# Optimization experiments

Measured on AMD Instinct MI355X. Metric: run time of the kernel, lower is better.

Reference implementation:

```python
import jax, jax.numpy as jnp
import numpy as np

NUM_HEADS = 16
HEAD_DIM = 64
HIDDEN = NUM_HEADS * HEAD_DIM
LN_EPS = 1e-6


def setup_inputs() -> dict:
    key = jax.random.key(0)
    ks = jax.random.split(key, 5)
    B, T, H = 2, 2048, HIDDEN
    s = 1.0 / np.sqrt(H)
    return {
        "h": jax.random.normal(ks[0], (B, T, H), jnp.float32),
        "Wq": jax.random.normal(ks[1], (H, H), jnp.float32) * s,
        "bq": jnp.zeros((H,), jnp.float32),
        "Wk": jax.random.normal(ks[2], (H, H), jnp.float32) * s,
        "bk": jnp.zeros((H,), jnp.float32),
        "Wv": jax.random.normal(ks[3], (H, H), jnp.float32) * s,
        "bv": jnp.zeros((H,), jnp.float32),
        "Wo": jax.random.normal(ks[4], (H, H), jnp.float32) * s,
        "bo": jnp.zeros((H,), jnp.float32),
        "gamma": jnp.ones((H,), jnp.float32),
        "beta": jnp.zeros((H,), jnp.float32),
    }


def _split_heads(x):
    B, T, H = x.shape
    return x.reshape(B, T, NUM_HEADS, HEAD_DIM).transpose(0, 2, 1, 3)  # [B,h,T,d]


def reference(h, Wq, bq, Wk, bk, Wv, bv, Wo, bo, gamma, beta):
    # QKV projections (nn.Linear: x @ W^T + b)
    Q = _split_heads(h @ Wq.T + bq)
    K = _split_heads(h @ Wk.T + bk)
    V = _split_heads(h @ Wv.T + bv)
    scale = HEAD_DIM ** -0.5
    scores = jnp.einsum("bhqd,bhkd->bhqk", Q, K) * scale  # [B,h,T,T]
    attn = jax.nn.softmax(scores, axis=-1)
    ctx = jnp.einsum("bhqk,bhkd->bhqd", attn, V)          # [B,h,T,d]
    B, _, T, _ = ctx.shape
    ctx = ctx.transpose(0, 2, 1, 3).reshape(B, T, HIDDEN)
    out = ctx @ Wo.T + bo + h  # dropout is identity at eval
    # LayerNorm(eps=1e-6)
    mu = out.mean(-1, keepdims=True)
    var = jnp.mean((out - mu) ** 2, -1, keepdims=True)
    return (out - mu) * jax.lax.rsqrt(var + LN_EPS) * gamma + beta
```

## Files before the change

kernel.cpp:

```cpp
#include <hip/hip_runtime.h>
#include <hip/hip_bf16.h>

#define NH   16
#define HD   64
#define HID  1024
#define TSEQ 2048
#define BATCH 2
#define KSCALE 0.18033688011112042f

typedef __attribute__((ext_vector_type(4))) float f32x4;
typedef __attribute__((ext_vector_type(8))) short s16x8;
typedef __attribute__((ext_vector_type(4))) short s16x4;
typedef __attribute__((ext_vector_type(8))) _Float16 f16x8;
typedef __attribute__((ext_vector_type(4))) _Float16 f16x4;
typedef __attribute__((ext_vector_type(2))) _Float16 f16x2;

__device__ __forceinline__ unsigned short f2bf(float f) {
  union { float f; unsigned int u; } v; v.f = f;
  unsigned int r = v.u + 0x7fffu + ((v.u >> 16) & 1u);
  return (unsigned short)(r >> 16);
}
__device__ __forceinline__ float bf2f(unsigned short b) {
  union { unsigned int u; float f; } v; v.u = ((unsigned int)b) << 16; return v.f;
}

__device__ __forceinline__ void gll16(const void* g, void* l) {
  __builtin_amdgcn_global_load_lds(
      (const __attribute__((address_space(1))) unsigned int*)g,
      (__attribute__((address_space(3))) unsigned int*)l, 16, 0, 0);
}

#define WAITBAR(N)                                                      \
  do {                                                                  \
    __builtin_amdgcn_sched_barrier(0);                                  \
    asm volatile("s_waitcnt vmcnt(" #N ")\n\ts_barrier" ::: "memory");  \
  } while (0)

__global__ __launch_bounds__(256) void cast_all_k(
    const float* __restrict__ h,
    const float* __restrict__ w0, const float* __restrict__ w1,
    const float* __restrict__ w2, const float* __restrict__ w3,
    unsigned short* __restrict__ hb, unsigned short* __restrict__ wbase) {
  int i = blockIdx.x * 256 + threadIdx.x;
  const float* src; unsigned short* dst; int idx; float sc = 1.f;
  if (i < 1048576) { src = h; dst = hb; idx = i; }
  else {
    int idx4 = i - 1048576;
    int w = idx4 >> 18;
    idx = idx4 & 262143;
    src = (w == 0) ? w0 : (w == 1) ? w1 : (w == 2) ? w2 : w3;
    dst = wbase + (size_t)(idx4 - idx) * 4;
    if (w == 1) sc = KSCALE;
  }
  float4 v = ((const float4*)src)[idx];
  ushort4 o;
  o.x = f2bf(v.x * sc); o.y = f2bf(v.y * sc); o.z = f2bf(v.z * sc); o.w = f2bf(v.w * sc);
  ((ushort4*)dst)[idx] = o;
}

__global__ __launch_bounds__(256) void gemm_qkv(
    const unsigned short* __restrict__ hb,
    const unsigned short* __restrict__ wcat,
    const float* __restrict__ bq, const float* __restrict__ bk, const float* __restrict__ bv,
    unsigned short* __restrict__ qo, unsigned short* __restrict__ ko,
    unsigned short* __restrict__ vto) {
  __shared__ unsigned short Ash[4][128 * 32];
  __shared__ unsigned short Bsh[4][192 * 32];
  const int tid = threadIdx.x, lane = tid & 63, wave = tid >> 6;
  const int l15 = lane & 15, quad = lane >> 4;
  const int wr = wave >> 1, wc = wave & 1;
  const int bn = blockIdx.x * 192, bm = blockIdx.y * 128;
  const char* Ab = (const char*)(hb + (size_t)bm * HID);
  const char* Bb = (const char*)(wcat + (size_t)bn * HID);
  const int off = tid * 16;
  const int r0 = off >> 6, c0 = off & 63;
  const size_t ga0 = (size_t)r0 * (HID * 2) + c0;
  const size_t ga1 = ga0 + (size_t)64  * (HID * 2);
  const size_t gb2 = ga0 + (size_t)128 * (HID * 2);
  const int lb0 = wave * 512;
  const int lb1 = 2048 + wave * 512;
  const int lb2 = 4096 + wave * 512;

  f32x4 acc[4][6];
#pragma unroll
  for (int i = 0; i < 4; ++i)
#pragma unroll
    for (int j = 0; j < 6; ++j) acc[i][j] = f32x4{0.f, 0.f, 0.f, 0.f};

  auto stage = [&](int bufi, int k0) {
    const size_t kb = (size_t)k0 * 2;
    gll16(Ab + ga0 + kb, &Ash[bufi][lb0]);
    gll16(Ab + ga1 + kb, &Ash[bufi][lb1]);
    gll16(Bb + ga0 + kb, &Bsh[bufi][lb0]);
    gll16(Bb + ga1 + kb, &Bsh[bufi][lb1]);
    gll16(Bb + gb2 + kb, &Bsh[bufi][lb2]);
  };
  auto compute = [&](int bufi) {
    s16x8 af[4], bfr[6];
#pragma unroll
    for (int i = 0; i < 4; ++i)
      af[i] = *(const s16x8*)(&Ash[bufi][(wr * 64 + i * 16 + l15) * 32 + quad * 8]);
#pragma unroll
    for (int j = 0; j < 6; ++j)
      bfr[j] = *(const s16x8*)(&Bsh[bufi][(wc * 96 + j * 16 + l15) * 32 + quad * 8]);
#pragma unroll
    for (int i = 0; i < 4; ++i)
#pragma unroll
      for (int j = 0; j < 6; ++j)
        acc[i][j] = __builtin_amdgcn_mfma_f32_16x16x32_bf16(af[i], bfr[j], acc[i][j], 0, 0, 0);
  };

  stage(0, 0);
  stage(1, 32);
  stage(2, 64);
  int cur = 0, pf = 3;
  const int NT = HID / 32;
  for (int t = 0; t < NT - 3; ++t) {
    WAITBAR(10);
    stage(pf, (t + 3) * 32);
    compute(cur);
    cur = (cur + 1) & 3;
    pf  = (pf + 1) & 3;
  }
  WAITBAR(10); compute(cur); cur = (cur + 1) & 3;
  WAITBAR(5);  compute(cur); cur = (cur + 1) & 3;
  WAITBAR(0);  compute(cur);

  const int rbase = bm + wr * 64;
#pragma unroll
  for (int j = 0; j < 6; ++j) {
    const int cg  = bn + wc * 96 + j * 16;
    const int mat = cg >> 10;
    const int coln = (cg & 1023) + l15;
    const int head = coln >> 6, d = coln & 63;
    if (mat == 2) {
      const float bb = bv[coln];
#pragma unroll
      for (int i = 0; i < 4; ++i) {
        const int row0 = rbase + i * 16 + quad * 4;
        const int bI = row0 >> 11, t0 = row0 & 2047;
        unsigned short o[4];
#pragma unroll
        for (int r = 0; r < 4; ++r) {
          _Float16 hv = (_Float16)(acc[i][j][r] + bb);
          o[r] = __builtin_bit_cast(unsigned short, hv);
        }
        *(s16x4*)(vto + ((size_t)((bI * NH + head) * HD + d)) * TSEQ + t0) = *(const s16x4*)o;
      }
    } else {
      unsigned short* dst = (mat == 0) ? qo : ko;
      const float bb = (mat == 0) ? bq[coln] : bk[coln] * KSCALE;
#pragma unroll
      for (int i = 0; i < 4; ++i) {
#pragma unroll
        for (int r = 0; r < 4; ++r) {
          const int row = rbase + i * 16 + quad * 4 + r;
          const int bI = row >> 11, t = row & 2047;
          dst[(((size_t)(bI * NH + head) * TSEQ) + t) * HD + d] = f2bf(acc[i][j][r] + bb);
        }
      }
    }
  }
}

__global__ __launch_bounds__(256) void gemm_out(
    const unsigned short* __restrict__ ctx, const unsigned short* __restrict__ wo,
    const float* __restrict__ bo, const float* __restrict__ hres,
    float* __restrict__ outf) {
  __shared__ unsigned short Ash[5][128 * 32];
  __shared__ unsigned short Bsh[5][64 * 32];
  const int tid = threadIdx.x, lane = tid & 63, wave = tid >> 6;
  const int l15 = lane & 15, quad = lane >> 4;
  const int wr = wave >> 1, wc = wave & 1;
  const int bn = blockIdx.x * 64, bm = blockIdx.y * 128;
  const char* Ab = (const char*)(ctx + (size_t)bm * HID);
  const char* Bb = (const char*)(wo + (size_t)bn * HID);
  const int off = tid * 16;
  const int r0 = off >> 6, c0 = off & 63;
  const size_t ga0 = (size_t)r0 * (HID * 2) + c0;
  const size_t ga1 = ga0 + (size_t)64 * (HID * 2);
  const int lb0 = wave * 512, lb1 = 2048 + wave * 512;

  f32x4 acc[4][2];
#pragma unroll
  for (int i = 0; i < 4; ++i)
#pragma unroll
    for (int j = 0; j < 2; ++j) acc[i][j] = f32x4{0.f, 0.f, 0.f, 0.f};

  auto stage = [&](int bufi, int k0) {
    const size_t kb = (size_t)k0 * 2;
    gll16(Ab + ga0 + kb, &Ash[bufi][lb0]);
    gll16(Ab + ga1 + kb, &Ash[bufi][lb1]);
    gll16(Bb + ga0 + kb, &Bsh[bufi][lb0]);
  };
  auto compute = [&](int bufi) {
    s16x8 af[4], bfr[2];
#pragma unroll
    for (int i = 0; i < 4; ++i)
      af[i] = *(const s16x8*)(&Ash[bufi][(wr * 64 + i * 16 + l15) * 32 + quad * 8]);
#pragma unroll
    for (int j = 0; j < 2; ++j)
      bfr[j] = *(const s16x8*)(&Bsh[bufi][(wc * 32 + j * 16 + l15) * 32 + quad * 8]);
#pragma unroll
    for (int i = 0; i < 4; ++i)
#pragma unroll
      for (int j = 0; j < 2; ++j)
        acc[i][j] = __builtin_amdgcn_mfma_f32_16x16x32_bf16(af[i], bfr[j], acc[i][j], 0, 0, 0);
  };

  stage(0, 0);
  stage(1, 32);
  stage(2, 64);
  stage(3, 96);
  int cur = 0, pf = 4;
  const int NT = HID / 32;
  for (int t = 0; t < NT - 4; ++t) {
    WAITBAR(9);
    stage(pf, (t + 4) * 32);
    compute(cur);
    cur = (cur == 4) ? 0 : cur + 1;
    pf  = (pf  == 4) ? 0 : pf + 1;
  }
  WAITBAR(9); compute(cur); cur = (cur == 4) ? 0 : cur + 1;
  WAITBAR(6); compute(cur); cur = (cur == 4) ? 0 : cur + 1;
  WAITBAR(3); compute(cur); cur = (cur == 4) ? 0 : cur + 1;
  WAITBAR(0); compute(cur);

#pragma unroll
  for (int j = 0; j < 2; ++j) {
    const int col = bn + wc * 32 + j * 16 + l15;
    const float bb = bo[col];
#pragma unroll
    for (int i = 0; i < 4; ++i) {
#pragma unroll
      for (int r = 0; r < 4; ++r) {
        const int row = bm + wr * 64 + i * 16 + quad * 4 + r;
        const size_t o = (size_t)row * HID + col;
        outf[o] = acc[i][j][r] + bb + hres[o];
      }
    }
  }
}

__global__ __launch_bounds__(256, 2) void attn_k(
    const unsigned short* __restrict__ qb, const unsigned short* __restrict__ kb,
    const unsigned short* __restrict__ vt, unsigned short* __restrict__ ctx,
    unsigned short* __restrict__ Opart, float* __restrict__ rsumP,
    int lsplit, int ntiles) {
  __shared__ unsigned short Ksh[64 * 72];
  __shared__ unsigned short Vsh[64 * 72];

  const int tid = threadIdx.x, lane = tid & 63, wave = tid >> 6;
  const int l15 = lane & 15, quad = lane >> 4;
  const int z = blockIdx.z;
  const int b = z >> lsplit;
  const int part = z & ((1 << lsplit) - 1);
  const int h = blockIdx.y, qt = blockIdx.x;
  const size_t ho = ((size_t)(b * NH + h)) * TSEQ * HD;
  const unsigned short* Qh = qb + ho;
  const unsigned short* Kh = kb + ho;
  const unsigned short* Vh = vt + ho;
  const int q0 = qt * 128 + wave * 32;
  const int kt0 = part * ntiles;

  s16x8 qf[2][2];
#pragma unroll
  for (int s = 0; s < 2; ++s)
#pragma unroll
    for (int ks = 0; ks < 2; ++ks)
      qf[s][ks] = *(const s16x8*)(Qh + (size_t)(q0 + s * 16 + l15) * HD + ks * 32 + quad * 8);

  f32x4 accO[4][2];
  float rsum[2];
#pragma unroll
  for (int n2 = 0; n2 < 4; ++n2)
#pragma unroll
    for (int s = 0; s < 2; ++s) accO[n2][s] = f32x4{0.f, 0.f, 0.f, 0.f};
  rsum[0] = rsum[1] = 0.f;

  const int sr = tid >> 3, sc = (tid & 7) * 8;
  const int c = tid & 7;
  const int vwb = (c >> 2) * 32 + (c & 1) * 16 + ((c & 3) >> 1) * 4;
  s16x8 kreg[2], vreg[2];
#pragma unroll
  for (int hf = 0; hf < 2; ++hf) {
    kreg[hf] = *(const s16x8*)(Kh + (size_t)(kt0 * 64 + sr + hf * 32) * HD + sc);
    vreg[hf] = *(const s16x8*)(Vh + (size_t)(sr + hf * 32) * TSEQ + kt0 * 64 + sc);
  }

  for (int kt = 0; kt < ntiles; ++kt) {
    __syncthreads();
#pragma unroll
    for (int hf = 0; hf < 2; ++hf) {
      *(s16x8*)(Ksh + (sr + hf * 32) * 72 + sc) = kreg[hf];
      const s16x4* vh = (const s16x4*)&vreg[hf];
      *(s16x4*)(Vsh + (sr + hf * 32) * 72 + vwb)     = vh[0];
      *(s16x4*)(Vsh + (sr + hf * 32) * 72 + vwb + 8) = vh[1];
    }
    __syncthreads();
    if (kt + 1 < ntiles) {
      const int k0n = (kt0 + kt + 1) * 64;
#pragma unroll
      for (int hf = 0; hf < 2; ++hf) {
        kreg[hf] = *(const s16x8*)(Kh + (size_t)(k0n + sr + hf * 32) * HD + sc);
        vreg[hf] = *(const s16x8*)(Vh + (size_t)(sr + hf * 32) * TSEQ + k0n + sc);
      }
    }

    f32x4 accS[2][4];
#pragma unroll
    for (int s = 0; s < 2; ++s)
#pragma unroll
      for (int n = 0; n < 4; ++n) accS[s][n] = f32x4{0.f, 0.f, 0.f, 0.f};
#pragma unroll
    for (int ks = 0; ks < 2; ++ks) {
#pragma unroll
      for (int n = 0; n < 4; ++n) {
        s16x8 kf = *(const s16x8*)(Ksh + (n * 16 + l15) * 72 + ks * 32 + quad * 8);
#pragma unroll
        for (int s = 0; s < 2; ++s)
          accS[s][n] = __builtin_amdgcn_mfma_f32_16x16x32_bf16(kf, qf[s][ks], accS[s][n], 0, 0, 0);
      }
    }

    f16x4 pB[2][4];
#pragma unroll
    for (int s = 0; s < 2; ++s)
#pragma unroll
      for (int n = 0; n < 4; ++n) {
        float e0 = __builtin_amdgcn_exp2f(accS[s][n][0]);
        float e1 = __builtin_amdgcn_exp2f(accS[s][n][1]);
        float e2 = __builtin_amdgcn_exp2f(accS[s][n][2]);
        float e3 = __builtin_amdgcn_exp2f(accS[s][n][3]);
        rsum[s] += (e0 + e1) + (e2 + e3);
        f16x2 lo = __builtin_bit_cast(f16x2, __builtin_amdgcn_cvt_pkrtz(e0, e1));
        f16x2 hi = __builtin_bit_cast(f16x2, __builtin_amdgcn_cvt_pkrtz(e2, e3));
        pB[s][n] = f16x4{lo[0], lo[1], hi[0], hi[1]};
      }

#pragma unroll
    for (int kk = 0; kk < 2; ++kk) {
      union { f16x4 h[2]; f16x8 v8; } u0, u1;
      u0.h[0] = pB[0][2 * kk]; u0.h[1] = pB[0][2 * kk + 1];
      u1.h[0] = pB[1][2 * kk]; u1.h[1] = pB[1][2 * kk + 1];
#pragma unroll
      for (int n2 = 0; n2 < 4; ++n2) {
        f16x8 vA = *(const f16x8*)(Vsh + (n2 * 16 + l15) * 72 + kk * 32 + quad * 8);
        accO[n2][0] = __builtin_amdgcn_mfma_f32_16x16x32_f16(vA, u0.v8, accO[n2][0], 0, 0, 0);
        accO[n2][1] = __builtin_amdgcn_mfma_f32_16x16x32_f16(vA, u1.v8, accO[n2][1], 0, 0, 0);
      }
    }
  }

#pragma unroll
  for (int s = 0; s < 2; ++s) {
    float t = rsum[s];
    t += __shfl_xor(t, 16, 64);
    t += __shfl_xor(t, 32, 64);
    rsum[s] = t;
  }

  if (lsplit) {
    const int slot = (part * BATCH + b) * NH + h;
    const size_t ob = (size_t)slot * TSEQ * HD;
#pragma unroll
    for (int s = 0; s < 2; ++s) {
      const int t = q0 + s * 16 + l15;
#pragma unroll
      for (int n2 = 0; n2 < 4; ++n2) {
        const int d0 = n2 * 16 + quad * 4;
        unsigned short o[4];
#pragma unroll
        for (int r = 0; r < 4; ++r) o[r] = f2bf(accO[n2][s][r]);
        *(s16x4*)(Opart + ob + (size_t)t * HD + d0) = *(const s16x4*)o;
      }
    }
    if (quad == 0) {
      const size_t rb = (size_t)slot * TSEQ;
#pragma unroll
      for (int s = 0; s < 2; ++s)
        rsumP[rb + q0 + s * 16 + l15] = rsum[s];
    }
  } else {
#pragma unroll
    for (int s = 0; s < 2; ++s) {
      const int t = q0 + s * 16 + l15;
      const float inv = 1.f / rsum[s];
#pragma unroll
      for (int n2 = 0; n2 < 4; ++n2) {
        const int d0 = n2 * 16 + quad * 4;
        unsigned short o[4];
#pragma unroll
        for (int r = 0; r < 4; ++r) o[r] = f2bf(accO[n2][s][r] * inv);
        *(s16x4*)(ctx + ((size_t)(b * TSEQ + t)) * HID + h * HD + d0) = *(const s16x4*)o;
      }
    }
  }
}

__global__ __launch_bounds__(256) void combine_k(
    const unsigned short* __restrict__ Opart, const float* __restrict__ rsumP,
    unsigned short* __restrict__ ctx, int nparts) {
  const int gtid = blockIdx.x * 256 + threadIdx.x;
  const int d = (gtid & 7) * 8;
  const int rem = gtid >> 3;
  const int t = rem & 2047;
  const int bh = rem >> 11;
  float acc[8] = {0, 0, 0, 0, 0, 0, 0, 0};
  float rs = 0.f;
  for (int p = 0; p < nparts; ++p) {
    const int slot = p * 32 + bh;
    s16x8 a = *(const s16x8*)(Opart + ((size_t)slot * TSEQ + t) * HD + d);
#pragma unroll
    for (int j = 0; j < 8; ++j) acc[j] += bf2f(((const unsigned short*)&a)[j]);
    rs += rsumP[(size_t)slot * TSEQ + t];
  }
  const float inv = 1.f / rs;
  unsigned short o[8];
#pragma unroll
  for (int j = 0; j < 8; ++j) o[j] = f2bf(acc[j] * inv);
  const int b = bh >> 4, h = bh & 15;
  *(s16x8*)(ctx + ((size_t)(b * TSEQ + t)) * HID + h * HD + d) = *(const s16x8*)o;
}

__global__ __launch_bounds__(256) void ln_k(float* __restrict__ io,
                                            const float* __restrict__ gamma,
                                            const float* __restrict__ beta) {
  const int row = blockIdx.x, tid = threadIdx.x;
  float x[4]; float s = 0.f, s2 = 0.f;
#pragma unroll
  for (int i = 0; i < 4; ++i) {
    x[i] = io[(size_t)row * HID + tid + i * 256];
    s += x[i]; s2 += x[i] * x[i];
  }
#pragma unroll
  for (int off = 1; off < 64; off <<= 1) {
    s  += __shfl_xor(s, off, 64);
    s2 += __shfl_xor(s2, off, 64);
  }
  __shared__ float red[8];
  const int wave = tid >> 6;
  if ((tid & 63) == 0) { red[wave] = s; red[wave + 4] = s2; }
  __syncthreads();
  s  = red[0] + red[1] + red[2] + red[3];
  s2 = red[4] + red[5] + red[6] + red[7];
  const float mean = s * (1.f / HID);
  const float var  = s2 * (1.f / HID) - mean * mean;
  const float rstd = rsqrtf(var + 1e-6f);
#pragma unroll
  for (int i = 0; i < 4; ++i) {
    const int col = tid + i * 256;
    io[(size_t)row * HID + col] = (x[i] - mean) * rstd * gamma[col] + beta[col];
  }
}

extern "C" void kernel_launch(void* const* d_in, const int* in_sizes, int n_in,
                              void* d_out, int out_size, void* d_ws, size_t ws_size,
                              hipStream_t stream) {
  const float* h    = (const float*)d_in[0];
  const float* Wq   = (const float*)d_in[1];
  const float* bq   = (const float*)d_in[2];
  const float* Wk   = (const float*)d_in[3];
  const float* bk   = (const float*)d_in[4];
  const float* Wv   = (const float*)d_in[5];
  const float* bv   = (const float*)d_in[6];
  const float* Wo   = (const float*)d_in[7];
  const float* bo   = (const float*)d_in[8];
  const float* gamma = (const float*)d_in[9];
  const float* beta  = (const float*)d_in[10];
  float* out = (float*)d_out;

  unsigned short* hb   = (unsigned short*)d_ws;
  unsigned short* wqb  = hb  + 4194304;
  unsigned short* wkb  = wqb + 1048576;
  unsigned short* wvb  = wkb + 1048576;
  unsigned short* wob  = wvb + 1048576;
  unsigned short* qb   = wob + 1048576;
  unsigned short* kb   = qb  + 4194304;
  unsigned short* vtf  = kb  + 4194304;
  unsigned short* Opart = vtf + 4194304;
  unsigned short* ctxb = hb;

  const size_t base = (size_t)(vtf + 4194304 - hb) * 2;
  int lsplit = 0;
  if (ws_size >= base + 2u * 8388608 + 2u * 262144) lsplit = 1;
  const int nparts = 1 << lsplit;
  float* rsumP = (float*)(Opart + (size_t)nparts * 4194304);

  cast_all_k<<<8192, 256, 0, stream>>>(h, Wq, Wk, Wv, Wo, hb, wqb);
  gemm_qkv<<<dim3(16, 32), 256, 0, stream>>>(hb, wqb, bq, bk, bv, qb, kb, vtf);
  attn_k<<<dim3(TSEQ / 128, NH, BATCH << lsplit), 256, 0, stream>>>(
      qb, kb, vtf, ctxb, Opart, rsumP, lsplit, 32 >> lsplit);
  if (lsplit)
    combine_k<<<2048, 256, 0, stream>>>(Opart, rsumP, ctxb, nparts);
  gemm_out<<<dim3(16, 32), 256, 0, stream>>>(ctxb, wob, bo, h, out);
  ln_k<<<4096, 256, 0, stream>>>(out, gamma, beta);
}
```

Before: 209.5 us.

## Software-pipeline attention loop with triple-buffered LDS and MFMA row sums

Restructures the attention inner loop into a software pipeline. QK^T for tile t+1 is issued alongside PV for tile t, using three rotating K/V LDS buffers so only one barrier per iteration is needed. The softmax row sum now comes from an extra MFMA against a ones vector instead of scalar adds plus cross-lane shuffles. LDS use triples to about 55KB per block, which may cut occupancy below the launch bound of two blocks. The row sums are also accumulated from fp16-rounded probabilities, which slightly changes precision.

After: 204.3 us. -2.5%, faster.

```diff
diff --git a/kernel.cpp b/kernel.cpp
--- a/kernel.cpp
+++ b/kernel.cpp
@@ -247,8 +247,8 @@
     const unsigned short* __restrict__ vt, unsigned short* __restrict__ ctx,
     unsigned short* __restrict__ Opart, float* __restrict__ rsumP,
     int lsplit, int ntiles) {
-  __shared__ unsigned short Ksh[64 * 72];
-  __shared__ unsigned short Vsh[64 * 72];
+  __shared__ unsigned short Ksh[3][64 * 72];
+  __shared__ unsigned short Vsh[3][64 * 72];
 
   const int tid = threadIdx.x, lane = tid & 63, wave = tid >> 6;
   const int l15 = lane & 15, quad = lane >> 4;
@@ -271,43 +271,42 @@
       qf[s][ks] = *(const s16x8*)(Qh + (size_t)(q0 + s * 16 + l15) * HD + ks * 32 + quad * 8);
 
   f32x4 accO[4][2];
-  float rsum[2];
+  f32x4 accR[2];
 #pragma unroll
   for (int n2 = 0; n2 < 4; ++n2)
 #pragma unroll
     for (int s = 0; s < 2; ++s) accO[n2][s] = f32x4{0.f, 0.f, 0.f, 0.f};
-  rsum[0] = rsum[1] = 0.f;
+  accR[0] = accR[1] = f32x4{0.f, 0.f, 0.f, 0.f};
+  const f16x8 vones = {(_Float16)1.f, (_Float16)1.f, (_Float16)1.f, (_Float16)1.f,
+                       (_Float16)1.f, (_Float16)1.f, (_Float16)1.f, (_Float16)1.f};
 
   const int sr = tid >> 3, sc = (tid & 7) * 8;
   const int c = tid & 7;
   const int vwb = (c >> 2) * 32 + (c & 1) * 16 + ((c & 3) >> 1) * 4;
   s16x8 kreg[2], vreg[2];
-#pragma unroll
-  for (int hf = 0; hf < 2; ++hf) {
-    kreg[hf] = *(const s16x8*)(Kh + (size_t)(kt0 * 64 + sr + hf * 32) * HD + sc);
-    vreg[hf] = *(const s16x8*)(Vh + (size_t)(sr + hf * 32) * TSEQ + kt0 * 64 + sc);
-  }
-
-  for (int kt = 0; kt < ntiles; ++kt) {
-    __syncthreads();
+
+  auto ldregs = [&](int kt) {
+    const int k0n = (kt0 + kt) * 64;
 #pragma unroll
     for (int hf = 0; hf < 2; ++hf) {
-      *(s16x8*)(Ksh + (sr + hf * 32) * 72 + sc) = kreg[hf];
+      kreg[hf] = *(const s16x8*)(Kh + (size_t)(k0n + sr + hf * 32) * HD + sc);
+      vreg[hf] = *(const s16x8*)(Vh + (size_t)(sr + hf * 32) * TSEQ + k0n + sc);
+    }
+  };
+  auto wlds = [&](int bi) {
+#pragma unroll
+    for (int hf = 0; hf < 2; ++hf) {
+      *(s16x8*)(Ksh[bi] + (sr + hf * 32) * 72 + sc) = kreg[hf];
       const s16x4* vh = (const s16x4*)&vreg[hf];
-      *(s16x4*)(Vsh + (sr + hf * 32) * 72 + vwb)     = vh[0];
-      *(s16x4*)(Vsh + (sr + hf * 32) * 72 + vwb + 8) = vh[1];
-    }
-    __syncthreads();
-    if (kt + 1 < ntiles) {
-      const int k0n = (kt0 + kt + 1) * 64;
-#pragma unroll
-      for (int hf = 0; hf < 2; ++hf) {
-        kreg[hf] = *(const s16x8*)(Kh + (size_t)(k0n + sr + hf * 32) * HD + sc);
-        vreg[hf] = *(const s16x8*)(Vh + (size_t)(sr + hf * 32) * TSEQ + k0n + sc);
-      }
-    }
-
-    f32x4 accS[2][4];
+      *(s16x4*)(Vsh[bi] + (sr + hf * 32) * 72 + vwb)     = vh[0];
+      *(s16x4*)(Vsh[bi] + (sr + hf * 32) * 72 + vwb + 8) = vh[1];
+    }
+  };
+
+  f32x4 accS[2][4];
+  f16x4 pP[2][4];
+
+  auto qkt = [&](int bi) {
 #pragma unroll
     for (int s = 0; s < 2; ++s)
 #pragma unroll
@@ -316,14 +315,14 @@
     for (int ks = 0; ks < 2; ++ks) {
 #pragma unroll
       for (int n = 0; n < 4; ++n) {
-        s16x8 kf = *(const s16x8*)(Ksh + (n * 16 + l15) * 72 + ks * 32 + quad * 8);
+        s16x8 kf = *(const s16x8*)(Ksh[bi] + (n * 16 + l15) * 72 + ks * 32 + quad * 8);
 #pragma unroll
         for (int s = 0; s < 2; ++s)
           accS[s][n] = __builtin_amdgcn_mfma_f32_16x16x32_bf16(kf, qf[s][ks], accS[s][n], 0, 0, 0);
       }
     }
-
-    f16x4 pB[2][4];
+  };
+  auto expp = [&]() {
 #pragma unroll
     for (int s = 0; s < 2; ++s)
 #pragma unroll
@@ -332,33 +331,48 @@
         float e1 = __builtin_amdgcn_exp2f(accS[s][n][1]);
         float e2 = __builtin_amdgcn_exp2f(accS[s][n][2]);
         float e3 = __builtin_amdgcn_exp2f(accS[s][n][3]);
-        rsum[s] += (e0 + e1) + (e2 + e3);
         f16x2 lo = __builtin_bit_cast(f16x2, __builtin_amdgcn_cvt_pkrtz(e0, e1));
         f16x2 hi = __builtin_bit_cast(f16x2, __builtin_amdgcn_cvt_pkrtz(e2, e3));
-        pB[s][n] = f16x4{lo[0], lo[1], hi[0], hi[1]};
-      }
-
+        pP[s][n] = f16x4{lo[0], lo[1], hi[0], hi[1]};
+      }
+  };
+  auto pv = [&](int bi) {
 #pragma unroll
     for (int kk = 0; kk < 2; ++kk) {
       union { f16x4 h[2]; f16x8 v8; } u0, u1;
-      u0.h[0] = pB[0][2 * kk]; u0.h[1] = pB[0][2 * kk + 1];
-      u1.h[0] = pB[1][2 * kk]; u1.h[1] = pB[1][2 * kk + 1];
+      u0.h[0] = pP[0][2 * kk]; u0.h[1] = pP[0][2 * kk + 1];
+      u1.h[0] = pP[1][2 * kk]; u1.h[1] = pP[1][2 * kk + 1];
+      accR[0] = __builtin_amdgcn_mfma_f32_16x16x32_f16(vones, u0.v8, accR[0], 0, 0, 0);
+      accR[1] = __builtin_amdgcn_mfma_f32_16x16x32_f16(vones, u1.v8, accR[1], 0, 0, 0);
 #pragma unroll
       for (int n2 = 0; n2 < 4; ++n2) {
-        f16x8 vA = *(const f16x8*)(Vsh + (n2 * 16 + l15) * 72 + kk * 32 + quad * 8);
+        f16x8 vA = *(const f16x8*)(Vsh[bi] + (n2 * 16 + l15) * 72 + kk * 32 + quad * 8);
         accO[n2][0] = __builtin_amdgcn_mfma_f32_16x16x32_f16(vA, u0.v8, accO[n2][0], 0, 0, 0);
         accO[n2][1] = __builtin_amdgcn_mfma_f32_16x16x32_f16(vA, u1.v8, accO[n2][1], 0, 0, 0);
       }
     }
-  }
-
-#pragma unroll
-  for (int s = 0; s < 2; ++s) {
-    float t = rsum[s];
-    t += __shfl_xor(t, 16, 64);
-    t += __shfl_xor(t, 32, 64);
-    rsum[s] = t;
-  }
+  };
+
+  ldregs(0);
+  wlds(0);
+  __syncthreads();
+  if (ntiles > 1) ldregs(1);
+  qkt(0);
+  expp();
+
+  int b0 = 0, b1 = 1;
+  for (int t = 0; t < ntiles - 1; ++t) {
+    wlds(b1);
+    __syncthreads();
+    if (t + 2 < ntiles) ldregs(t + 2);
+    qkt(b1);
+    pv(b0);
+    expp();
+    b0 = b1; b1 = (b1 == 2) ? 0 : b1 + 1;
+  }
+  pv(b0);
+
+  float rsum[2] = {accR[0][0], accR[1][0]};
 
   if (lsplit) {
     const int slot = (part * BATCH + b) * NH + h;
```
